# Kernel tuning notes

Measured on AMD Instinct MI355X. Metric: run time of the kernel, lower is better.

## Reference

```python
import jax, jax.numpy as jnp
import numpy as np


def setup_inputs() -> dict:
    key = jax.random.key(0)
    k1, k2, k3, k4 = jax.random.split(key, 4)
    B, T, E, H = 16, 2048, 1024, 128
    x = jax.random.normal(k1, (B, T, E), dtype=jnp.float32)
    Wk = jax.random.normal(k2, (E, H), dtype=jnp.float32) * (E ** -0.5)
    Wq = jax.random.normal(k3, (E, H), dtype=jnp.float32) * (E ** -0.5)
    Wv = jax.random.normal(k4, (E, H), dtype=jnp.float32) * (E ** -0.5)
    return {"x": x, "Wk": Wk, "Wq": Wq, "Wv": Wv}


def reference(x, Wk, Wq, Wv):
    # x: [B,T,E]; Wk/Wq/Wv: [E,H]
    B, T, E = x.shape
    H = Wk.shape[1]
    k = jnp.einsum('bte,eh->bth', x, Wk)
    q = jnp.einsum('bte,eh->bth', x, Wq)
    v = jnp.einsum('bte,eh->bth', x, Wv)
    # scores [B,T,T]; original masks with -inf THEN scales (equivalent math)
    scores = jnp.einsum('bqh,bkh->bqk', q, k) * (H ** -0.5)
    causal = jnp.tril(jnp.ones((T, T), dtype=bool))
    scores = jnp.where(causal, scores, -jnp.inf)
    weights = jax.nn.softmax(scores, axis=-1)
    # dropout disabled (eval mode reference)
    return jnp.einsum('bqk,bkh->bqh', weights, v)
```

## Files before the change

kernel.cpp:

```cpp
#include <hip/hip_runtime.h>

#define B_ 16
#define T_ 2048
#define E_ 1024
#define H_ 128

typedef short bf16x8 __attribute__((ext_vector_type(8)));
typedef float f32x4 __attribute__((ext_vector_type(4)));
typedef unsigned short u16x4 __attribute__((ext_vector_type(4)));

static __device__ __forceinline__ unsigned short f2bf(float f) {
    unsigned int u = __float_as_uint(f);
    u += 0x7FFFu + ((u >> 16) & 1u);
    return (unsigned short)(u >> 16);
}
static __device__ __forceinline__ unsigned int pk2(unsigned short a, unsigned short b) {
    return (unsigned int)a | ((unsigned int)b << 16);
}
static __device__ __forceinline__ bf16x8 frag(uint4 v) {
    return __builtin_bit_cast(bf16x8, v);
}
static __device__ __forceinline__ void gl16(const unsigned short* g, unsigned short* l) {
    __builtin_amdgcn_global_load_lds(
        (const __attribute__((address_space(1))) void*)g,
        (__attribute__((address_space(3))) void*)l, 16, 0, 0);
}

__global__ __launch_bounds__(256) void cvt_kernel(
    const float* __restrict__ x,
    const float* __restrict__ w0, const float* __restrict__ w1,
    const float* __restrict__ w2,
    unsigned short* __restrict__ xb, unsigned short* __restrict__ wt)
{
    if (blockIdx.x < 16384) {
        size_t i = ((size_t)blockIdx.x * 256 + threadIdx.x) * 8;
        float4 a = *(const float4*)(x + i);
        float4 b = *(const float4*)(x + i + 4);
        uint4 o;
        o.x = pk2(f2bf(a.x), f2bf(a.y));
        o.y = pk2(f2bf(a.z), f2bf(a.w));
        o.z = pk2(f2bf(b.x), f2bf(b.y));
        o.w = pk2(f2bf(b.z), f2bf(b.w));
        *(uint4*)(xb + i) = o;
    } else {
        int g   = (blockIdx.x - 16384) * 256 + threadIdx.x;
        int arr = g >> 14;
        int rem = g & 16383;
        int h   = rem >> 7;
        int e0  = (rem & 127) * 8;
        const float* src = (arr == 0) ? w0 : (arr == 1) ? w1 : w2;
        unsigned short b[8];
#pragma unroll
        for (int i = 0; i < 8; i++) b[i] = f2bf(src[(size_t)(e0 + i) * H_ + h]);
        uint4 o;
        o.x = pk2(b[0], b[1]); o.y = pk2(b[2], b[3]);
        o.z = pk2(b[4], b[5]); o.w = pk2(b[6], b[7]);
        *(uint4*)&wt[(size_t)(arr * 128 + h) * E_ + e0] = o;
    }
}

__global__ __launch_bounds__(256, 3) void proj_kernel(
    const unsigned short* __restrict__ xb,
    const unsigned short* __restrict__ wt,
    unsigned short* __restrict__ q_ws,
    unsigned short* __restrict__ kp_ws,
    unsigned short* __restrict__ vt_ws)
{
    const int m0 = blockIdx.x * 128;
    const int by = blockIdx.y;
    __shared__ __align__(16) unsigned short As[128 * 32];
    __shared__ __align__(16) unsigned short Bs[128 * 32];

    const int tid  = threadIdx.x;
    const int lane = tid & 63;
    const int w    = tid >> 6;
    const int quad = lane >> 4;
    const int lm   = lane & 15;
    const int rw   = (w & 1) * 64;
    const int cw   = (w >> 1) * 64;

    const int srow = w * 32 + (lane >> 2);
    const int sch  = (lane & 3) * 8;
    const unsigned short* ga0 = xb + (size_t)(m0 + srow) * E_ + sch;
    const unsigned short* ga1 = ga0 + (size_t)16 * E_;
    const unsigned short* gb0 = wt + (size_t)(by * 128 + srow) * E_ + sch;
    const unsigned short* gb1 = gb0 + (size_t)16 * E_;
    unsigned short* la0 = As + (size_t)(w * 2)     * 512;
    unsigned short* la1 = As + (size_t)(w * 2 + 1) * 512;
    unsigned short* lb0 = Bs + (size_t)(w * 2)     * 512;
    unsigned short* lb1 = Bs + (size_t)(w * 2 + 1) * 512;

    const f32x4 z4 = {0.f, 0.f, 0.f, 0.f};
    f32x4 acc[4][4];
#pragma unroll
    for (int i = 0; i < 4; i++)
#pragma unroll
        for (int j = 0; j < 4; j++) acc[i][j] = z4;

    for (int kb = 0; kb < 32; kb++) {
        __syncthreads();
        gl16(ga0, la0); gl16(ga1, la1);
        gl16(gb0, lb0); gl16(gb1, lb1);
        __syncthreads();
        ga0 += 32; ga1 += 32; gb0 += 32; gb1 += 32;

        bf16x8 a[4], b[4];
#pragma unroll
        for (int am = 0; am < 4; am++)
            a[am] = frag(*(const uint4*)&As[(rw + am * 16 + lm) * 32 + quad * 8]);
#pragma unroll
        for (int bn = 0; bn < 4; bn++)
            b[bn] = frag(*(const uint4*)&Bs[(cw + bn * 16 + lm) * 32 + quad * 8]);
#pragma unroll
        for (int am = 0; am < 4; am++)
#pragma unroll
            for (int bn = 0; bn < 4; bn++)
                acc[am][bn] = __builtin_amdgcn_mfma_f32_16x16x32_bf16(
                    a[am], b[bn], acc[am][bn], 0, 0, 0);
    }

    const int bb = m0 >> 11;
    const int t0 = m0 & 2047;
#pragma unroll
    for (int am = 0; am < 4; am++)
#pragma unroll
        for (int bn = 0; bn < 4; bn++) {
            const int col = cw + bn * 16 + lm;
            if (by == 0) {
                const int row = m0 + rw + am * 16 + quad * 4;
#pragma unroll
                for (int r = 0; r < 4; r++)
                    q_ws[(size_t)(row + r) * H_ + col] = f2bf(acc[am][bn][r]);
            } else if (by == 1) {
                const int tl = t0 + rw + am * 16 + quad * 4;
#pragma unroll
                for (int r = 0; r < 4; r++) {
                    int t = tl + r;
                    kp_ws[(size_t)(bb * 64 + (t >> 5)) * 4096 +
                          (col >> 5) * 1024 + (t & 31) * 32 + (col & 31)] =
                        f2bf(acc[am][bn][r]);
                }
            } else {
                const int tt = t0 + rw + am * 16 + quad * 4;
                u16x4 p;
#pragma unroll
                for (int r = 0; r < 4; r++) p[r] = f2bf(acc[am][bn][r]);
                *(u16x4*)&vt_ws[((size_t)(bb * 64 + (tt >> 5)) * 128 + col) * 32 + (tt & 31)] = p;
            }
        }
}

__global__ __launch_bounds__(256, 2) void attn_kernel(
    const unsigned short* __restrict__ q_ws,
    const unsigned short* __restrict__ kp_ws,
    const unsigned short* __restrict__ vt_ws,
    float* __restrict__ out)
{
    __shared__ __align__(16) unsigned short Ks[2][4096];
    __shared__ __align__(16) unsigned short Vs[2][4096];
    __shared__ __align__(16) unsigned short Ps[4][16][40];

    const int batch = blockIdx.x & 15;
    const int p     = blockIdx.x >> 4;

    const int tid  = threadIdx.x;
    const int lane = tid & 63;
    const int ww   = tid >> 6;
    const int quad = lane >> 4;
    const int lm   = lane & 15;
    const float scale = 0.08838834764831845f;

    bf16x8 ones;
#pragma unroll
    for (int i = 0; i < 8; i++) ones[i] = (short)0x3F80;
    const f32x4 z4 = {0.f, 0.f, 0.f, 0.f};

    const size_t bq = (size_t)batch * T_ * H_;
    const int so = ww * 1024 + lane * 8;
    const unsigned short* Kt = kp_ws + (size_t)(batch * 64) * 4096 + so;
    const unsigned short* Vt = vt_ws + (size_t)(batch * 64) * 4096 + so;

#pragma unroll 1
    for (int pi = 0; pi < 2; pi++) {
        const int tau = pi ? (31 - p) : p;
        const int nkt = 2 * tau + 2;

        bf16x8 qf[4];
#pragma unroll
        for (int h = 0; h < 4; h++)
            qf[h] = frag(*(const uint4*)(q_ws + bq +
                     (size_t)(tau * 64 + ww * 16 + lm) * H_ + h * 32 + quad * 8));

        f32x4 o[9];
#pragma unroll
        for (int f = 0; f < 9; f++) o[f] = z4;

        gl16(Kt, &Ks[0][ww * 1024]); gl16(Kt + 512, &Ks[0][ww * 1024 + 512]);
        gl16(Vt, &Vs[0][ww * 1024]); gl16(Vt + 512, &Vs[0][ww * 1024 + 512]);

        for (int kt = 0; kt < nkt; kt++) {
            const int cb = kt & 1;
            __syncthreads();

            if (kt + 1 < nkt) {
                const int nb = cb ^ 1;
                const unsigned short* kg = Kt + (size_t)(kt + 1) * 4096;
                const unsigned short* vg = Vt + (size_t)(kt + 1) * 4096;
                gl16(kg, &Ks[nb][ww * 1024]); gl16(kg + 512, &Ks[nb][ww * 1024 + 512]);
                gl16(vg, &Vs[nb][ww * 1024]); gl16(vg + 512, &Vs[nb][ww * 1024 + 512]);
            }

            f32x4 st0 = z4, st1 = z4;
#pragma unroll
            for (int h = 0; h < 4; h++) {
                bf16x8 kf0 = frag(*(const uint4*)&Ks[cb][(h * 32 + lm) * 32 + quad * 8]);
                bf16x8 kf1 = frag(*(const uint4*)&Ks[cb][(h * 32 + 16 + lm) * 32 + quad * 8]);
                st0 = __builtin_amdgcn_mfma_f32_16x16x32_bf16(kf0, qf[h], st0, 0, 0, 0);
                st1 = __builtin_amdgcn_mfma_f32_16x16x32_bf16(kf1, qf[h], st1, 0, 0, 0);
            }

            const int qg = tau * 64 + ww * 16 + lm;
            const int k0 = kt * 32;
            u16x4 pa, pb;
#pragma unroll
            for (int r = 0; r < 4; r++) {
                int kv0 = k0 + quad * 4 + r;
                float e0 = __expf(st0[r] * scale);
                float e1 = __expf(st1[r] * scale);
                pa[r] = (kv0      <= qg) ? f2bf(e0) : (unsigned short)0;
                pb[r] = (kv0 + 16 <= qg) ? f2bf(e1) : (unsigned short)0;
            }
            *(u16x4*)&Ps[ww][lm][quad * 4]      = pa;
            *(u16x4*)&Ps[ww][lm][16 + quad * 4] = pb;
            bf16x8 pf = frag(*(const uint4*)&Ps[ww][lm][quad * 8]);

#pragma unroll
            for (int f = 0; f < 8; f++) {
                bf16x8 vfr = frag(*(const uint4*)&Vs[cb][(f * 16 + lm) * 32 + quad * 8]);
                o[f] = __builtin_amdgcn_mfma_f32_16x16x32_bf16(pf, vfr, o[f], 0, 0, 0);
            }
            o[8] = __builtin_amdgcn_mfma_f32_16x16x32_bf16(pf, ones, o[8], 0, 0, 0);
        }

        float* op = out + bq + (size_t)(tau * 64 + ww * 16) * H_;
#pragma unroll
        for (int r = 0; r < 4; r++) {
            float inv = 1.f / o[8][r];
#pragma unroll
            for (int f = 0; f < 8; f++)
                op[(size_t)(quad * 4 + r) * H_ + f * 16 + lm] = o[f][r] * inv;
        }
        __syncthreads();
    }
}

extern "C" void kernel_launch(void* const* d_in, const int* in_sizes, int n_in,
                              void* d_out, int out_size, void* d_ws, size_t ws_size,
                              hipStream_t stream)
{
    const float* x  = (const float*)d_in[0];
    const float* Wk = (const float*)d_in[1];
    const float* Wq = (const float*)d_in[2];
    const float* Wv = (const float*)d_in[3];
    float* out = (float*)d_out;

    const size_t MH = (size_t)B_ * T_ * H_;
    const size_t ME = (size_t)B_ * T_ * E_;
    unsigned short* q_ws  = (unsigned short*)d_ws;
    unsigned short* kp_ws = q_ws + MH;
    unsigned short* vt_ws = kp_ws + MH;
    unsigned short* wt    = vt_ws + MH;
    unsigned short* xb    = wt + (size_t)384 * E_;

    cvt_kernel<<<dim3(16576), dim3(256), 0, stream>>>(x, Wq, Wk, Wv, xb, wt);
    proj_kernel<<<dim3(256, 3), dim3(256), 0, stream>>>(xb, wt, q_ws, kp_ws, vt_ws);
    attn_kernel<<<dim3(256), dim3(256), 0, stream>>>(q_ws, kp_ws, vt_ws, out);
}
```

Baseline: 298.9 us.

## Fuse x bf16 conversion into projection GEMM and split attention blocks

The separate fp32-to-bf16 pass over x is removed. The projection kernel now loads fp32 x directly, converts it in registers and writes it to double-buffered LDS. It also computes Q, K and V together in one 512-thread block with a 128x384 tile, so x is read only once, and the next K-slice is prefetched while the MFMAs run. The attention kernel launches 512 blocks, one causal tile each, instead of 256 blocks that each looped over a balanced pair of tiles; this trades explicit load balancing for more parallelism. The aim is to cut a large bf16 round-trip of x through memory, at the cost of higher LDS and register use in the projection kernel.

Result: faster. 281.2 us (-5.9%).

```diff
diff --git a/kernel.cpp b/kernel.cpp
--- a/kernel.cpp
+++ b/kernel.cpp
@@ -26,126 +26,135 @@
         (__attribute__((address_space(3))) void*)l, 16, 0, 0);
 }
 
-__global__ __launch_bounds__(256) void cvt_kernel(
+__global__ __launch_bounds__(256) void cvtw_kernel(
+    const float* __restrict__ w0, const float* __restrict__ w1,
+    const float* __restrict__ w2, unsigned short* __restrict__ wt)
+{
+    int g   = blockIdx.x * 256 + threadIdx.x;
+    int arr = g >> 14;
+    int rem = g & 16383;
+    int h   = rem >> 7;
+    int e0  = (rem & 127) * 8;
+    const float* src = (arr == 0) ? w0 : (arr == 1) ? w1 : w2;
+    unsigned short b[8];
+#pragma unroll
+    for (int i = 0; i < 8; i++) b[i] = f2bf(src[(size_t)(e0 + i) * H_ + h]);
+    uint4 o;
+    o.x = pk2(b[0], b[1]); o.y = pk2(b[2], b[3]);
+    o.z = pk2(b[4], b[5]); o.w = pk2(b[6], b[7]);
+    *(uint4*)&wt[(size_t)(arr * 128 + h) * E_ + e0] = o;
+}
+
+__global__ __launch_bounds__(512, 2) void proj_kernel(
     const float* __restrict__ x,
-    const float* __restrict__ w0, const float* __restrict__ w1,
-    const float* __restrict__ w2,
-    unsigned short* __restrict__ xb, unsigned short* __restrict__ wt)
-{
-    if (blockIdx.x < 16384) {
-        size_t i = ((size_t)blockIdx.x * 256 + threadIdx.x) * 8;
-        float4 a = *(const float4*)(x + i);
-        float4 b = *(const float4*)(x + i + 4);
-        uint4 o;
-        o.x = pk2(f2bf(a.x), f2bf(a.y));
-        o.y = pk2(f2bf(a.z), f2bf(a.w));
-        o.z = pk2(f2bf(b.x), f2bf(b.y));
-        o.w = pk2(f2bf(b.z), f2bf(b.w));
-        *(uint4*)(xb + i) = o;
-    } else {
-        int g   = (blockIdx.x - 16384) * 256 + threadIdx.x;
-        int arr = g >> 14;
-        int rem = g & 16383;
-        int h   = rem >> 7;
-        int e0  = (rem & 127) * 8;
-        const float* src = (arr == 0) ? w0 : (arr == 1) ? w1 : w2;
-        unsigned short b[8];
-#pragma unroll
-        for (int i = 0; i < 8; i++) b[i] = f2bf(src[(size_t)(e0 + i) * H_ + h]);
-        uint4 o;
-        o.x = pk2(b[0], b[1]); o.y = pk2(b[2], b[3]);
-        o.z = pk2(b[4], b[5]); o.w = pk2(b[6], b[7]);
-        *(uint4*)&wt[(size_t)(arr * 128 + h) * E_ + e0] = o;
-    }
-}
-
-__global__ __launch_bounds__(256, 3) void proj_kernel(
-    const unsigned short* __restrict__ xb,
     const unsigned short* __restrict__ wt,
     unsigned short* __restrict__ q_ws,
     unsigned short* __restrict__ kp_ws,
     unsigned short* __restrict__ vt_ws)
 {
     const int m0 = blockIdx.x * 128;
-    const int by = blockIdx.y;
-    __shared__ __align__(16) unsigned short As[128 * 32];
-    __shared__ __align__(16) unsigned short Bs[128 * 32];
+    __shared__ __align__(16) unsigned short As[2][128 * 32];
+    __shared__ __align__(16) unsigned short Bs[2][384 * 32];
 
     const int tid  = threadIdx.x;
     const int lane = tid & 63;
     const int w    = tid >> 6;
     const int quad = lane >> 4;
     const int lm   = lane & 15;
-    const int rw   = (w & 1) * 64;
-    const int cw   = (w >> 1) * 64;
-
-    const int srow = w * 32 + (lane >> 2);
-    const int sch  = (lane & 3) * 8;
-    const unsigned short* ga0 = xb + (size_t)(m0 + srow) * E_ + sch;
-    const unsigned short* ga1 = ga0 + (size_t)16 * E_;
-    const unsigned short* gb0 = wt + (size_t)(by * 128 + srow) * E_ + sch;
-    const unsigned short* gb1 = gb0 + (size_t)16 * E_;
-    unsigned short* la0 = As + (size_t)(w * 2)     * 512;
-    unsigned short* la1 = As + (size_t)(w * 2 + 1) * 512;
-    unsigned short* lb0 = Bs + (size_t)(w * 2)     * 512;
-    unsigned short* lb1 = Bs + (size_t)(w * 2 + 1) * 512;
+    const int wr   = (w >> 2) * 64;
+    const int wc   = (w & 3) * 96;
+
+    const int srow = tid >> 2;
+    const int scol = (tid & 3) * 8;
+    const float* gx = x + (size_t)(m0 + srow) * E_ + scol;
+    const unsigned short* gw = wt + (size_t)srow * E_ + scol;
 
     const f32x4 z4 = {0.f, 0.f, 0.f, 0.f};
-    f32x4 acc[4][4];
+    f32x4 acc[4][6];
 #pragma unroll
     for (int i = 0; i < 4; i++)
 #pragma unroll
-        for (int j = 0; j < 4; j++) acc[i][j] = z4;
+        for (int j = 0; j < 6; j++) acc[i][j] = z4;
+
+    auto stageB = [&](int kb, int buf) {
+        const unsigned short* g = gw + kb * 32;
+        unsigned short* l = &Bs[buf][tid * 8];
+        gl16(g,                    l);
+        gl16(g + (size_t)128 * E_, l + 4096);
+        gl16(g + (size_t)256 * E_, l + 8192);
+    };
+    auto writeA = [&](float4 a0, float4 a1, int buf) {
+        uint4 o;
+        o.x = pk2(f2bf(a0.x), f2bf(a0.y));
+        o.y = pk2(f2bf(a0.z), f2bf(a0.w));
+        o.z = pk2(f2bf(a1.x), f2bf(a1.y));
+        o.w = pk2(f2bf(a1.z), f2bf(a1.w));
+        *(uint4*)&As[buf][srow * 32 + scol] = o;
+    };
+
+    float4 a0 = *(const float4*)gx;
+    float4 a1 = *(const float4*)(gx + 4);
+    stageB(0, 0);
+    writeA(a0, a1, 0);
+    a0 = *(const float4*)(gx + 32);
+    a1 = *(const float4*)(gx + 36);
 
     for (int kb = 0; kb < 32; kb++) {
+        const int cb = kb & 1;
         __syncthreads();
-        gl16(ga0, la0); gl16(ga1, la1);
-        gl16(gb0, lb0); gl16(gb1, lb1);
-        __syncthreads();
-        ga0 += 32; ga1 += 32; gb0 += 32; gb1 += 32;
-
-        bf16x8 a[4], b[4];
+
+        const int kb2 = (kb + 2 < 32) ? kb + 2 : 31;
+        float4 n0 = *(const float4*)(gx + kb2 * 32);
+        float4 n1 = *(const float4*)(gx + kb2 * 32 + 4);
+        if (kb + 1 < 32) {
+            stageB(kb + 1, cb ^ 1);
+            writeA(a0, a1, cb ^ 1);
+        }
+
+        bf16x8 a[4], b[6];
 #pragma unroll
         for (int am = 0; am < 4; am++)
-            a[am] = frag(*(const uint4*)&As[(rw + am * 16 + lm) * 32 + quad * 8]);
-#pragma unroll
-        for (int bn = 0; bn < 4; bn++)
-            b[bn] = frag(*(const uint4*)&Bs[(cw + bn * 16 + lm) * 32 + quad * 8]);
+            a[am] = frag(*(const uint4*)&As[cb][(wr + am * 16 + lm) * 32 + quad * 8]);
+#pragma unroll
+        for (int bn = 0; bn < 6; bn++)
+            b[bn] = frag(*(const uint4*)&Bs[cb][(wc + bn * 16 + lm) * 32 + quad * 8]);
 #pragma unroll
         for (int am = 0; am < 4; am++)
 #pragma unroll
-            for (int bn = 0; bn < 4; bn++)
+            for (int bn = 0; bn < 6; bn++)
                 acc[am][bn] = __builtin_amdgcn_mfma_f32_16x16x32_bf16(
                     a[am], b[bn], acc[am][bn], 0, 0, 0);
+
+        a0 = n0; a1 = n1;
     }
 
-    const int bb = m0 >> 11;
-    const int t0 = m0 & 2047;
 #pragma unroll
     for (int am = 0; am < 4; am++)
 #pragma unroll
-        for (int bn = 0; bn < 4; bn++) {
-            const int col = cw + bn * 16 + lm;
-            if (by == 0) {
-                const int row = m0 + rw + am * 16 + quad * 4;
+        for (int bn = 0; bn < 6; bn++) {
+            const int gcol  = wc + bn * 16 + lm;
+            const int sel   = gcol >> 7;
+            const int c     = gcol & 127;
+            const int rbase = m0 + wr + am * 16 + quad * 4;
+            const int bb    = rbase >> 11;
+            const int t     = rbase & 2047;
+            if (sel == 0) {
 #pragma unroll
                 for (int r = 0; r < 4; r++)
-                    q_ws[(size_t)(row + r) * H_ + col] = f2bf(acc[am][bn][r]);
-            } else if (by == 1) {
-                const int tl = t0 + rw + am * 16 + quad * 4;
+                    q_ws[(size_t)(rbase + r) * H_ + c] = f2bf(acc[am][bn][r]);
+            } else if (sel == 1) {
 #pragma unroll
                 for (int r = 0; r < 4; r++) {
-                    int t = tl + r;
-                    kp_ws[(size_t)(bb * 64 + (t >> 5)) * 4096 +
-                          (col >> 5) * 1024 + (t & 31) * 32 + (col & 31)] =
+                    int tt = t + r;
+                    kp_ws[(size_t)(bb * 64 + (tt >> 5)) * 4096 +
+                          (c >> 5) * 1024 + (tt & 31) * 32 + (c & 31)] =
                         f2bf(acc[am][bn][r]);
                 }
             } else {
-                const int tt = t0 + rw + am * 16 + quad * 4;
-                u16x4 p;
-#pragma unroll
-                for (int r = 0; r < 4; r++) p[r] = f2bf(acc[am][bn][r]);
-                *(u16x4*)&vt_ws[((size_t)(bb * 64 + (tt >> 5)) * 128 + col) * 32 + (tt & 31)] = p;
+                u16x4 pv;
+#pragma unroll
+                for (int r = 0; r < 4; r++) pv[r] = f2bf(acc[am][bn][r]);
+                *(u16x4*)&vt_ws[((size_t)(bb * 64 + (t >> 5)) * 128 + c) * 32 + (t & 31)] = pv;
             }
         }
 }
@@ -160,8 +169,11 @@
     __shared__ __align__(16) unsigned short Vs[2][4096];
     __shared__ __align__(16) unsigned short Ps[4][16][40];
 
-    const int batch = blockIdx.x & 15;
-    const int p     = blockIdx.x >> 4;
+    const int bid   = blockIdx.x;
+    const int batch = bid & 15;
+    const int p     = (bid >> 4) & 15;
+    const int tau   = (bid >> 8) ? (31 - p) : p;
+    const int nkt   = 2 * tau + 2;
 
     const int tid  = threadIdx.x;
     const int lane = tid & 63;
@@ -180,77 +192,70 @@
     const unsigned short* Kt = kp_ws + (size_t)(batch * 64) * 4096 + so;
     const unsigned short* Vt = vt_ws + (size_t)(batch * 64) * 4096 + so;
 
-#pragma unroll 1
-    for (int pi = 0; pi < 2; pi++) {
-        const int tau = pi ? (31 - p) : p;
-        const int nkt = 2 * tau + 2;
-
-        bf16x8 qf[4];
-#pragma unroll
-        for (int h = 0; h < 4; h++)
-            qf[h] = frag(*(const uint4*)(q_ws + bq +
-                     (size_t)(tau * 64 + ww * 16 + lm) * H_ + h * 32 + quad * 8));
-
-        f32x4 o[9];
-#pragma unroll
-        for (int f = 0; f < 9; f++) o[f] = z4;
-
-        gl16(Kt, &Ks[0][ww * 1024]); gl16(Kt + 512, &Ks[0][ww * 1024 + 512]);
-        gl16(Vt, &Vs[0][ww * 1024]); gl16(Vt + 512, &Vs[0][ww * 1024 + 512]);
-
-        for (int kt = 0; kt < nkt; kt++) {
-            const int cb = kt & 1;
-            __syncthreads();
-
-            if (kt + 1 < nkt) {
-                const int nb = cb ^ 1;
-                const unsigned short* kg = Kt + (size_t)(kt + 1) * 4096;
-                const unsigned short* vg = Vt + (size_t)(kt + 1) * 4096;
-                gl16(kg, &Ks[nb][ww * 1024]); gl16(kg + 512, &Ks[nb][ww * 1024 + 512]);
-                gl16(vg, &Vs[nb][ww * 1024]); gl16(vg + 512, &Vs[nb][ww * 1024 + 512]);
-            }
-
-            f32x4 st0 = z4, st1 = z4;
-#pragma unroll
-            for (int h = 0; h < 4; h++) {
-                bf16x8 kf0 = frag(*(const uint4*)&Ks[cb][(h * 32 + lm) * 32 + quad * 8]);
-                bf16x8 kf1 = frag(*(const uint4*)&Ks[cb][(h * 32 + 16 + lm) * 32 + quad * 8]);
-                st0 = __builtin_amdgcn_mfma_f32_16x16x32_bf16(kf0, qf[h], st0, 0, 0, 0);
-                st1 = __builtin_amdgcn_mfma_f32_16x16x32_bf16(kf1, qf[h], st1, 0, 0, 0);
-            }
-
-            const int qg = tau * 64 + ww * 16 + lm;
-            const int k0 = kt * 32;
-            u16x4 pa, pb;
-#pragma unroll
-            for (int r = 0; r < 4; r++) {
-                int kv0 = k0 + quad * 4 + r;
-                float e0 = __expf(st0[r] * scale);
-                float e1 = __expf(st1[r] * scale);
-                pa[r] = (kv0      <= qg) ? f2bf(e0) : (unsigned short)0;
-                pb[r] = (kv0 + 16 <= qg) ? f2bf(e1) : (unsigned short)0;
-            }
-            *(u16x4*)&Ps[ww][lm][quad * 4]      = pa;
-            *(u16x4*)&Ps[ww][lm][16 + quad * 4] = pb;
-            bf16x8 pf = frag(*(const uint4*)&Ps[ww][lm][quad * 8]);
-
-#pragma unroll
-            for (int f = 0; f < 8; f++) {
-                bf16x8 vfr = frag(*(const uint4*)&Vs[cb][(f * 16 + lm) * 32 + quad * 8]);
-                o[f] = __builtin_amdgcn_mfma_f32_16x16x32_bf16(pf, vfr, o[f], 0, 0, 0);
-            }
-            o[8] = __builtin_amdgcn_mfma_f32_16x16x32_bf16(pf, ones, o[8], 0, 0, 0);
-        }
-
-        float* op = out + bq + (size_t)(tau * 64 + ww * 16) * H_;
+    bf16x8 qf[4];
+#pragma unroll
+    for (int h = 0; h < 4; h++)
+        qf[h] = frag(*(const uint4*)(q_ws + bq +
+                 (size_t)(tau * 64 + ww * 16 + lm) * H_ + h * 32 + quad * 8));
+
+    f32x4 o[9];
+#pragma unroll
+    for (int f = 0; f < 9; f++) o[f] = z4;
+
+    gl16(Kt, &Ks[0][ww * 1024]); gl16(Kt + 512, &Ks[0][ww * 1024 + 512]);
+    gl16(Vt, &Vs[0][ww * 1024]); gl16(Vt + 512, &Vs[0][ww * 1024 + 512]);
+
+    for (int kt = 0; kt < nkt; kt++) {
+        const int cb = kt & 1;
+        __syncthreads();
+
+        if (kt + 1 < nkt) {
+            const int nb = cb ^ 1;
+            const unsigned short* kg = Kt + (size_t)(kt + 1) * 4096;
+            const unsigned short* vg = Vt + (size_t)(kt + 1) * 4096;
+            gl16(kg, &Ks[nb][ww * 1024]); gl16(kg + 512, &Ks[nb][ww * 1024 + 512]);
+            gl16(vg, &Vs[nb][ww * 1024]); gl16(vg + 512, &Vs[nb][ww * 1024 + 512]);
+        }
+
+        f32x4 st0 = z4, st1 = z4;
+#pragma unroll
+        for (int h = 0; h < 4; h++) {
+            bf16x8 kf0 = frag(*(const uint4*)&Ks[cb][(h * 32 + lm) * 32 + quad * 8]);
+            bf16x8 kf1 = frag(*(const uint4*)&Ks[cb][(h * 32 + 16 + lm) * 32 + quad * 8]);
+            st0 = __builtin_amdgcn_mfma_f32_16x16x32_bf16(kf0, qf[h], st0, 0, 0, 0);
+            st1 = __builtin_amdgcn_mfma_f32_16x16x32_bf16(kf1, qf[h], st1, 0, 0, 0);
+        }
+
+        const int qg = tau * 64 + ww * 16 + lm;
+        const int k0 = kt * 32;
+        u16x4 pa, pb;
 #pragma unroll
         for (int r = 0; r < 4; r++) {
-            float inv = 1.f / o[8][r];
-#pragma unroll
-            for (int f = 0; f < 8; f++)
-                op[(size_t)(quad * 4 + r) * H_ + f * 16 + lm] = o[f][r] * inv;
-        }
-        __syncthreads();
+            int kv0 = k0 + quad * 4 + r;
+            float e0 = __expf(st0[r] * scale);
+            float e1 = __expf(st1[r] * scale);
+            pa[r] = (kv0      <= qg) ? f2bf(e0) : (unsigned short)0;
+            pb[r] = (kv0 + 16 <= qg) ? f2bf(e1) : (unsigned short)0;
+        }
+        *(u16x4*)&Ps[ww][lm][quad * 4]      = pa;
+        *(u16x4*)&Ps[ww][lm][16 + quad * 4] = pb;
+        bf16x8 pf = frag(*(const uint4*)&Ps[ww][lm][quad * 8]);
+
+#pragma unroll
+        for (int f = 0; f < 8; f++) {
+            bf16x8 vfr = frag(*(const uint4*)&Vs[cb][(f * 16 + lm) * 32 + quad * 8]);
+            o[f] = __builtin_amdgcn_mfma_f32_16x16x32_bf16(pf, vfr, o[f], 0, 0, 0);
+        }
+        o[8] = __builtin_amdgcn_mfma_f32_16x16x32_bf16(pf, ones, o[8], 0, 0, 0);
+    }
+
+    float* op = out + bq + (size_t)(tau * 64 + ww * 16) * H_;
+#pragma unroll
+    for (int r = 0; r < 4; r++) {
+        float inv = 1.f / o[8][r];
+#pragma unroll
+        for (int f = 0; f < 8; f++)
+            op[(size_t)(quad * 4 + r) * H_ + f * 16 + lm] = o[f][r] * inv;
     }
 }
 
@@ -265,14 +270,12 @@
     float* out = (float*)d_out;
 
     const size_t MH = (size_t)B_ * T_ * H_;
-    const size_t ME = (size_t)B_ * T_ * E_;
     unsigned short* q_ws  = (unsigned short*)d_ws;
     unsigned short* kp_ws = q_ws + MH;
     unsigned short* vt_ws = kp_ws + MH;
     unsigned short* wt    = vt_ws + MH;
-    unsigned short* xb    = wt + (size_t)384 * E_;
-
-    cvt_kernel<<<dim3(16576), dim3(256), 0, stream>>>(x, Wq, Wk, Wv, xb, wt);
-    proj_kernel<<<dim3(256, 3), dim3(256), 0, stream>>>(xb, wt, q_ws, kp_ws, vt_ws);
-    attn_kernel<<<dim3(256), dim3(256), 0, stream>>>(q_ws, kp_ws, vt_ws, out);
-}
+
+    cvtw_kernel<<<dim3(192), dim3(256), 0, stream>>>(Wq, Wk, Wv, wt);
+    proj_kernel<<<dim3(256), dim3(512), 0, stream>>>(x, wt, q_ws, kp_ws, vt_ws);
+    attn_kernel<<<dim3(512), dim3(256), 0, stream>>>(q_ws, kp_ws, vt_ws, out);
+}
```

## Split attention query tiles across blocks and triple-buffer K/V loads

Applied to the files above, without the earlier changes.

Each block now handles a single query tile instead of a balanced pair, and the grid doubles to 512 blocks. The K/V staging becomes a 3-deep ring with explicit vmcnt waits and a raw s_barrier, prefetching two tiles ahead. s_setprio is raised around the MFMA sections. The aim is more parallelism and better hiding of load latency, at the cost of uneven per-block work (causal tile lengths vary) and more LDS per block.

After: 300.5 us. Within noise of the previous version (+0.5%).

```diff
diff --git a/kernel.cpp b/kernel.cpp
--- a/kernel.cpp
+++ b/kernel.cpp
@@ -156,12 +156,15 @@
     const unsigned short* __restrict__ vt_ws,
     float* __restrict__ out)
 {
-    __shared__ __align__(16) unsigned short Ks[2][4096];
-    __shared__ __align__(16) unsigned short Vs[2][4096];
+    __shared__ __align__(16) unsigned short Ks[3][4096];
+    __shared__ __align__(16) unsigned short Vs[3][4096];
     __shared__ __align__(16) unsigned short Ps[4][16][40];
 
-    const int batch = blockIdx.x & 15;
-    const int p     = blockIdx.x >> 4;
+    const int bid   = blockIdx.x;
+    const int batch = bid & 15;
+    const int p     = (bid >> 4) & 15;
+    const int tau   = (bid >> 8) ? (31 - p) : p;
+    const int nkt   = 2 * tau + 2;
 
     const int tid  = threadIdx.x;
     const int lane = tid & 63;
@@ -180,77 +183,81 @@
     const unsigned short* Kt = kp_ws + (size_t)(batch * 64) * 4096 + so;
     const unsigned short* Vt = vt_ws + (size_t)(batch * 64) * 4096 + so;
 
-#pragma unroll 1
-    for (int pi = 0; pi < 2; pi++) {
-        const int tau = pi ? (31 - p) : p;
-        const int nkt = 2 * tau + 2;
-
-        bf16x8 qf[4];
-#pragma unroll
-        for (int h = 0; h < 4; h++)
-            qf[h] = frag(*(const uint4*)(q_ws + bq +
-                     (size_t)(tau * 64 + ww * 16 + lm) * H_ + h * 32 + quad * 8));
-
-        f32x4 o[9];
-#pragma unroll
-        for (int f = 0; f < 9; f++) o[f] = z4;
-
-        gl16(Kt, &Ks[0][ww * 1024]); gl16(Kt + 512, &Ks[0][ww * 1024 + 512]);
-        gl16(Vt, &Vs[0][ww * 1024]); gl16(Vt + 512, &Vs[0][ww * 1024 + 512]);
-
-        for (int kt = 0; kt < nkt; kt++) {
-            const int cb = kt & 1;
-            __syncthreads();
-
-            if (kt + 1 < nkt) {
-                const int nb = cb ^ 1;
-                const unsigned short* kg = Kt + (size_t)(kt + 1) * 4096;
-                const unsigned short* vg = Vt + (size_t)(kt + 1) * 4096;
-                gl16(kg, &Ks[nb][ww * 1024]); gl16(kg + 512, &Ks[nb][ww * 1024 + 512]);
-                gl16(vg, &Vs[nb][ww * 1024]); gl16(vg + 512, &Vs[nb][ww * 1024 + 512]);
-            }
-
-            f32x4 st0 = z4, st1 = z4;
-#pragma unroll
-            for (int h = 0; h < 4; h++) {
-                bf16x8 kf0 = frag(*(const uint4*)&Ks[cb][(h * 32 + lm) * 32 + quad * 8]);
-                bf16x8 kf1 = frag(*(const uint4*)&Ks[cb][(h * 32 + 16 + lm) * 32 + quad * 8]);
-                st0 = __builtin_amdgcn_mfma_f32_16x16x32_bf16(kf0, qf[h], st0, 0, 0, 0);
-                st1 = __builtin_amdgcn_mfma_f32_16x16x32_bf16(kf1, qf[h], st1, 0, 0, 0);
-            }
-
-            const int qg = tau * 64 + ww * 16 + lm;
-            const int k0 = kt * 32;
-            u16x4 pa, pb;
-#pragma unroll
-            for (int r = 0; r < 4; r++) {
-                int kv0 = k0 + quad * 4 + r;
-                float e0 = __expf(st0[r] * scale);
-                float e1 = __expf(st1[r] * scale);
-                pa[r] = (kv0      <= qg) ? f2bf(e0) : (unsigned short)0;
-                pb[r] = (kv0 + 16 <= qg) ? f2bf(e1) : (unsigned short)0;
-            }
-            *(u16x4*)&Ps[ww][lm][quad * 4]      = pa;
-            *(u16x4*)&Ps[ww][lm][16 + quad * 4] = pb;
-            bf16x8 pf = frag(*(const uint4*)&Ps[ww][lm][quad * 8]);
-
-#pragma unroll
-            for (int f = 0; f < 8; f++) {
-                bf16x8 vfr = frag(*(const uint4*)&Vs[cb][(f * 16 + lm) * 32 + quad * 8]);
-                o[f] = __builtin_amdgcn_mfma_f32_16x16x32_bf16(pf, vfr, o[f], 0, 0, 0);
-            }
-            o[8] = __builtin_amdgcn_mfma_f32_16x16x32_bf16(pf, ones, o[8], 0, 0, 0);
-        }
-
-        float* op = out + bq + (size_t)(tau * 64 + ww * 16) * H_;
+    auto stage = [&](int t, int b) {
+        const unsigned short* kg = Kt + (size_t)t * 4096;
+        const unsigned short* vg = Vt + (size_t)t * 4096;
+        gl16(kg,       &Ks[b][ww * 1024]);
+        gl16(kg + 512, &Ks[b][ww * 1024 + 512]);
+        gl16(vg,       &Vs[b][ww * 1024]);
+        gl16(vg + 512, &Vs[b][ww * 1024 + 512]);
+    };
+
+    bf16x8 qf[4];
+#pragma unroll
+    for (int h = 0; h < 4; h++)
+        qf[h] = frag(*(const uint4*)(q_ws + bq +
+                 (size_t)(tau * 64 + ww * 16 + lm) * H_ + h * 32 + quad * 8));
+
+    f32x4 o[9];
+#pragma unroll
+    for (int f = 0; f < 9; f++) o[f] = z4;
+
+    stage(0, 0);
+    stage(1, 1);
+
+    for (int kt = 0; kt < nkt; kt++) {
+        const int cb = kt % 3;
+        asm volatile("s_waitcnt vmcnt(4) lgkmcnt(0)" ::: "memory");
+        __builtin_amdgcn_sched_barrier(0);
+        __builtin_amdgcn_s_barrier();
+        __builtin_amdgcn_sched_barrier(0);
+
+        int ks = kt + 2; if (ks > nkt - 1) ks = nkt - 1;
+        stage(ks, (kt + 2) % 3);
+
+        f32x4 st0 = z4, st1 = z4;
+        __builtin_amdgcn_s_setprio(1);
+#pragma unroll
+        for (int h = 0; h < 4; h++) {
+            bf16x8 kf0 = frag(*(const uint4*)&Ks[cb][(h * 32 + lm) * 32 + quad * 8]);
+            bf16x8 kf1 = frag(*(const uint4*)&Ks[cb][(h * 32 + 16 + lm) * 32 + quad * 8]);
+            st0 = __builtin_amdgcn_mfma_f32_16x16x32_bf16(kf0, qf[h], st0, 0, 0, 0);
+            st1 = __builtin_amdgcn_mfma_f32_16x16x32_bf16(kf1, qf[h], st1, 0, 0, 0);
+        }
+        __builtin_amdgcn_s_setprio(0);
+
+        const int qg = tau * 64 + ww * 16 + lm;
+        const int k0 = kt * 32;
+        u16x4 pa, pb;
 #pragma unroll
         for (int r = 0; r < 4; r++) {
-            float inv = 1.f / o[8][r];
-#pragma unroll
-            for (int f = 0; f < 8; f++)
-                op[(size_t)(quad * 4 + r) * H_ + f * 16 + lm] = o[f][r] * inv;
-        }
-        __syncthreads();
+            int kv0 = k0 + quad * 4 + r;
+            float e0 = __expf(st0[r] * scale);
+            float e1 = __expf(st1[r] * scale);
+            pa[r] = (kv0      <= qg) ? f2bf(e0) : (unsigned short)0;
+            pb[r] = (kv0 + 16 <= qg) ? f2bf(e1) : (unsigned short)0;
+        }
+        *(u16x4*)&Ps[ww][lm][quad * 4]      = pa;
+        *(u16x4*)&Ps[ww][lm][16 + quad * 4] = pb;
+        bf16x8 pf = frag(*(const uint4*)&Ps[ww][lm][quad * 8]);
+
+        __builtin_amdgcn_s_setprio(1);
+#pragma unroll
+        for (int f = 0; f < 8; f++) {
+            bf16x8 vfr = frag(*(const uint4*)&Vs[cb][(f * 16 + lm) * 32 + quad * 8]);
+            o[f] = __builtin_amdgcn_mfma_f32_16x16x32_bf16(pf, vfr, o[f], 0, 0, 0);
+        }
+        o[8] = __builtin_amdgcn_mfma_f32_16x16x32_bf16(pf, ones, o[8], 0, 0, 0);
+        __builtin_amdgcn_s_setprio(0);
+    }
+
+    float* op = out + bq + (size_t)(tau * 64 + ww * 16) * H_;
+#pragma unroll
+    for (int r = 0; r < 4; r++) {
+        float inv = 1.f / o[8][r];
+#pragma unroll
+        for (int f = 0; f < 8; f++)
+            op[(size_t)(quad * 4 + r) * H_ + f * 16 + lm] = o[f][r] * inv;
     }
 }
 
@@ -265,7 +272,6 @@
     float* out = (float*)d_out;
 
     const size_t MH = (size_t)B_ * T_ * H_;
-    const size_t ME = (size_t)B_ * T_ * E_;
     unsigned short* q_ws  = (unsigned short*)d_ws;
     unsigned short* kp_ws = q_ws + MH;
     unsigned short* vt_ws = kp_ws + MH;
@@ -274,5 +280,5 @@
 
     cvt_kernel<<<dim3(16576), dim3(256), 0, stream>>>(x, Wq, Wk, Wv, xb, wt);
     proj_kernel<<<dim3(256, 3), dim3(256), 0, stream>>>(xb, wt, q_ws, kp_ws, vt_ws);
-    attn_kernel<<<dim3(256), dim3(256), 0, stream>>>(q_ws, kp_ws, vt_ws, out);
-}
+    attn_kernel<<<dim3(512), dim3(256), 0, stream>>>(q_ws, kp_ws, vt_ws, out);
+}
```
